# Optimization experiments

Hardware: AMD Instinct MI355X
Metric: run time of the kernel (lower is better)

Reference implementation:

```python
import jax, jax.numpy as jnp
import numpy as np

B = 32768
EPS = 0.2  # BatchNorm eps used in the original module


def _xavier(key, shape):
    fan_in, fan_out = shape[-2], shape[-1]
    std = (2.0 / (fan_in + fan_out)) ** 0.5
    return (jax.random.normal(key, shape, jnp.float32) * std).astype(jnp.float32)


def bn(x, g, b):
    # training-mode BatchNorm1d: batch stats over the batch axis (-2), biased var
    m = jnp.mean(x, axis=-2, keepdims=True)
    v = jnp.mean(jnp.square(x - m), axis=-2, keepdims=True)
    return (x - m) * jax.lax.rsqrt(v + EPS) * g + b


def setup_inputs() -> dict:
    key = jax.random.key(0)
    ks = iter(jax.random.split(key, 48))
    inp = {}
    inp['x1f'] = jax.random.normal(next(ks), (B, 512), jnp.float32)
    inp['x2f'] = jax.random.normal(next(ks), (B, 512), jnp.float32)
    # shared trunk
    inp['W1'] = _xavier(next(ks), (512, 256)); inp['b1'] = jnp.zeros(256, jnp.float32)
    inp['W2'] = _xavier(next(ks), (256, 256)); inp['b2'] = jnp.zeros(256, jnp.float32)
    # batchnorm affine params (bn1:256, bn2:256, bn3:128, bn4:64)
    inp['g1'] = jnp.ones(256, jnp.float32); inp['be1'] = jnp.zeros(256, jnp.float32)
    inp['g2'] = jnp.ones(256, jnp.float32); inp['be2'] = jnp.zeros(256, jnp.float32)
    inp['g3'] = jnp.ones(128, jnp.float32); inp['be3'] = jnp.zeros(128, jnp.float32)
    inp['g4'] = jnp.ones(64, jnp.float32); inp['be4'] = jnp.zeros(64, jnp.float32)
    # 4 branch projections from each stream (x11..x14, x21..x24), stacked on axis 0
    inp['Wbx1'] = _xavier(next(ks), (4, 256, 256)); inp['bbx1'] = jnp.zeros((4, 256), jnp.float32)
    inp['Wbx2'] = _xavier(next(ks), (4, 256, 256)); inp['bbx2'] = jnp.zeros((4, 256), jnp.float32)
    # gating MLPs (xw*1, xw*2, xw*3, y*), stacked over the 4 attributes
    inp['Wwa'] = _xavier(next(ks), (4, 512, 128)); inp['bwa'] = jnp.zeros((4, 128), jnp.float32)
    inp['Wwb'] = _xavier(next(ks), (4, 128, 64)); inp['bwb'] = jnp.zeros((4, 64), jnp.float32)
    inp['Wwc'] = _xavier(next(ks), (4, 64, 64)); inp['bwc'] = jnp.zeros((4, 64), jnp.float32)
    inp['Wy'] = _xavier(next(ks), (4, 64, 2)); inp['by'] = jnp.zeros((4, 2), jnp.float32)
    # combine layers x1c..x4c, stacked
    inp['Wc'] = _xavier(next(ks), (4, 512, 256)); inp['bc'] = jnp.zeros((4, 256), jnp.float32)
    # output heads (different class counts: 3, 3, 6, 4)
    inp['Wo1'] = _xavier(next(ks), (256, 3)); inp['bo1'] = jnp.zeros(3, jnp.float32)
    inp['Wo2'] = _xavier(next(ks), (256, 3)); inp['bo2'] = jnp.zeros(3, jnp.float32)
    inp['Wo3'] = _xavier(next(ks), (256, 6)); inp['bo3'] = jnp.zeros(6, jnp.float32)
    inp['Wo4'] = _xavier(next(ks), (256, 4)); inp['bo4'] = jnp.zeros(4, jnp.float32)
    return inp


def reference(x1f, x2f, W1, b1, W2, b2, g1, be1, g2, be2, g3, be3, g4, be4,
              Wbx1, bbx1, Wbx2, bbx2, Wwa, bwa, Wwb, bwb, Wwc, bwc, Wy, by,
              Wc, bc, Wo1, bo1, Wo2, bo2, Wo3, bo3, Wo4, bo4):
    relu = jax.nn.relu

    def trunk(x):
        h = bn(relu(x @ W1 + b1), g1, be1)
        return bn(relu(h @ W2 + b2), g2, be2)

    h1 = trunk(x1f)  # [B,256]
    h2 = trunk(x2f)  # [B,256]

    # 4 branch features per stream, each bn1-normalized: [4,B,256]
    b1x = bn(relu(jnp.einsum('bi,kio->kbo', h1, Wbx1) + bbx1[:, None, :]), g1, be1)
    b2x = bn(relu(jnp.einsum('bi,kio->kbo', h2, Wbx2) + bbx2[:, None, :]), g1, be1)

    # gating MLP per attribute -> 2-way softmax weights
    xcat = jnp.concatenate([b1x, b2x], axis=-1)  # [4,B,512]
    a = bn(relu(jnp.einsum('kbi,kio->kbo', xcat, Wwa) + bwa[:, None, :]), g3, be3)
    b_ = bn(relu(jnp.einsum('kbi,kio->kbo', a, Wwb) + bwb[:, None, :]), g4, be4)
    c = bn(relu(jnp.einsum('kbi,kio->kbo', b_, Wwc) + bwc[:, None, :]), g4, be4)
    y = jax.nn.softmax(jnp.einsum('kbi,kio->kbo', c, Wy) + by[:, None, :], axis=-1)  # [4,B,2]

    # the original per-column loop == one broadcast multiply per stream
    xw = jnp.concatenate([b1x * y[..., 0:1], b2x * y[..., 1:2]], axis=-1)  # [4,B,512]

    # combine layers (dropout is identity in eval)
    xc = bn(relu(jnp.einsum('kbi,kio->kbo', xw, Wc) + bc[:, None, :]), g1, be1)  # [4,B,256]

    y1o = jax.nn.softmax(xc[0] @ Wo1 + bo1, axis=-1)
    y2o = jax.nn.softmax(xc[1] @ Wo2 + bo2, axis=-1)
    y3o = jax.nn.softmax(xc[2] @ Wo3 + bo3, axis=-1)
    y4o = jax.nn.softmax(xc[3] @ Wo4 + bo4, axis=-1)
    return (y1o, y2o, y3o, y4o)
```

## Files before the change

kernel.cpp:

```cpp
#include <hip/hip_runtime.h>
#include <hip/hip_bf16.h>


typedef unsigned short u16;
typedef _Float16 f16x8 __attribute__((ext_vector_type(8)));
typedef float f32x4 __attribute__((ext_vector_type(4)));

#define B_ROWS 32768
#define EPS_BN 0.2f
#define BINV (1.0f / 32768.0f)

__device__ __forceinline__ float bf2f(u16 u) {
    union { unsigned int i; float f; } c;
    c.i = ((unsigned int)u) << 16;
    return c.f;
}
__device__ __forceinline__ u16 f2bf(float f) {
    union { float f; unsigned int i; } c;
    c.f = f;
    unsigned int x = c.i;
    return (u16)((x + 0x7FFFu + ((x >> 16) & 1u)) >> 16);
}
__device__ __forceinline__ float h2f(u16 u) {
    _Float16 h;
    __builtin_memcpy(&h, &u, 2);
    return (float)h;
}
__device__ __forceinline__ u16 f2h(float f) {
    _Float16 h = (_Float16)f;
    u16 u;
    __builtin_memcpy(&u, &h, 2);
    return u;
}
__device__ __forceinline__ float ldp(const void* p, long i, int flag) {
    return flag ? bf2f(((const u16*)p)[i]) : ((const float*)p)[i];
}
__device__ __forceinline__ void gload16(const u16* gp, u16* lp) {
    __builtin_amdgcn_global_load_lds(
        (const __attribute__((address_space(1))) unsigned int*)gp,
        (__attribute__((address_space(3))) unsigned int*)lp, 16, 0, 0);
}

__global__ void detect_dtype(const u16* __restrict__ x, int* __restrict__ flag) {
    const int lane = threadIdx.x;
    const u16 v = x[2 * lane];
    const int e = (v >> 7) & 0xFF;
    const bool plausible = (e >= 110 && e <= 140);
    const unsigned long long m = __ballot(plausible);
    if (lane == 0) *flag = (__popcll(m) >= 58) ? 1 : 0;
}

struct PTab { const void* p[20]; int n[20]; int off[20]; };

__global__ void convert_params(PTab t, float* __restrict__ dst,
                               const int* __restrict__ flag) {
    const int ti = blockIdx.y;
    const int n = t.n[ti];
    float* o = dst + t.off[ti];
    const int isbf = *flag;
    for (int i = blockIdx.x * 256 + threadIdx.x; i < n; i += gridDim.x * 256)
        o[i] = ldp(t.p[ti], i, isbf);
}

__global__ __launch_bounds__(256) void prep_w(
    const void* __restrict__ W, long wstride,
    const void* __restrict__ bias, long bstride,
    const float* __restrict__ psum, const float* __restrict__ psq, int pstride,
    const void* __restrict__ pg, const void* __restrict__ pbe, int gmask,
    const int* __restrict__ dtflag,
    u16* __restrict__ Wt, long wtstride,
    float* __restrict__ biasP, float* __restrict__ T0o,
    float* __restrict__ T1o, float* __restrict__ bsum, long bost,
    int K, int khalf)
{
    const int tid = threadIdx.x;
    const int n = blockIdx.x;
    const int N = gridDim.x;
    const int inst = blockIdx.y;
    const int flag = *dtflag;
    __shared__ float sn[512], tn[512];
    __shared__ float r0[4], r1[4];

    for (int i = tid; i < K; i += 256) {
        float s = 1.f, t = 0.f;
        if (psum) {
            float m = psum[(long)pstride * inst + i] * BINV;
            float v = psq[(long)pstride * inst + i] * BINV - m * m;
            float g = ldp(pg, i & gmask, flag);
            float b = ldp(pbe, i & gmask, flag);
            s = g * rsqrtf(v + EPS_BN);
            t = b - m * s;
        }
        sn[i] = s; tn[i] = t;
    }
    __syncthreads();
    float p0 = 0.f, p1 = 0.f;
    for (int k = tid; k < K; k += 256) {
        float wv = ldp(W, wstride * inst + (long)k * N + n, flag);
        Wt[wtstride * inst + (long)n * K + k] = f2h(sn[k] * wv);
        float tw = tn[k] * wv;
        if (k < khalf) p0 += tw; else p1 += tw;
    }
#pragma unroll
    for (int off = 32; off; off >>= 1) {
        p0 += __shfl_xor(p0, off);
        p1 += __shfl_xor(p1, off);
    }
    const int lane = tid & 63, wid = tid >> 6;
    if (lane == 0) { r0[wid] = p0; r1[wid] = p1; }
    __syncthreads();
    if (tid == 0) {
        float t0 = r0[0] + r0[1] + r0[2] + r0[3];
        float t1 = r1[0] + r1[1] + r1[2] + r1[3];
        float bp = ldp(bias, bstride * inst + n, flag);
        long o = bost * inst + n;
        biasP[o] = bp; T0o[o] = t0; T1o[o] = t1; bsum[o] = bp + t0 + t1;
    }
}

__global__ __launch_bounds__(256) void reduce_stats(
    const float* __restrict__ part, int X, int colsPer,
    float* __restrict__ outS, float* __restrict__ outQ, int total)
{
    const int t = blockIdx.x * 256 + threadIdx.x;
    if (t >= total) return;
    const int p = t / colsPer, c = t % colsPer;
    const float* pb = part + (long)p * X * 2 * colsPer + c;
    float s = 0.f, q = 0.f;
#pragma unroll 4
    for (int x = 0; x < X; ++x) {
        s += pb[(long)x * 2 * colsPer];
        q += pb[(long)x * 2 * colsPer + colsPer];
    }
    outS[t] = s; outQ[t] = q;
}

template <bool XSTAGE, bool ROWW, int WM, int WN, int K>
__global__ __launch_bounds__(256, 3) void gemm_mfma(
    const void* __restrict__ X, const void* __restrict__ X2,
    long xstride, int ximask, int ldx, int ksplit, long ksecond,
    const int* __restrict__ dtflag,
    const u16* __restrict__ Wt, long wtstride,
    const float* __restrict__ biasP, const float* __restrict__ T0,
    const float* __restrict__ T1, const float* __restrict__ bsum, int bN,
    u16* __restrict__ Out, long ostride, int ldout,
    float* __restrict__ gsum, float* __restrict__ gsq, int sstride,
    float* __restrict__ part,
    const float* __restrict__ Y0v)
{
    const int tid = threadIdx.x;
    const int lane = tid & 63;
    const int wid = tid >> 6;
    const int wm = wid / WN, wn = wid % WN;
    const int inst = blockIdx.z;
    const int rowB = blockIdx.x * (64 * WM);
    const int nBase = blockIdx.y * (64 * WN);
    const int n0 = nBase + wn * 64;
    const int fm = lane & 15, quad = lane >> 4;
    const int rloc = lane >> 3;
    const int cg = (lane & 7) ^ rloc;

    __shared__ __align__(16) u16 As[WM * 4096];
    __shared__ __align__(16) u16 Bs[WN * 4096];
    __shared__ float redS[4][64];
    __shared__ float redQ[4][64];

    const bool xf32 = XSTAGE && (*dtflag == 0);
    const char* xb;
    if (XSTAGE) xb = (const char*)(inst == 0 ? X : X2);
    else        xb = (const char*)X + 2l * xstride * (inst & ximask);
    const u16* wtp = Wt + wtstride * inst;
    u16* op = Out + ostride * inst;

    f32x4 acc[4][4];
#pragma unroll
    for (int i = 0; i < 4; ++i)
#pragma unroll
        for (int j = 0; j < 4; ++j) acc[i][j] = (f32x4){0.f, 0.f, 0.f, 0.f};

    _Float16 ysc[2][4];
    if constexpr (ROWW) {
        const float* yp = Y0v + (long)inst * B_ROWS;
#pragma unroll
        for (int mi = 0; mi < 4; ++mi) {
            const float y = yp[rowB + wm * 64 + mi * 16 + fm];
            ysc[0][mi] = (_Float16)y;
            ysc[1][mi] = (_Float16)(1.f - y);
        }
    }

    for (int kt = 0; kt < K / 64; ++kt) {
        const int kk = kt * 64;
        __syncthreads();
        if constexpr (XSTAGE) {
#pragma unroll
            for (int p = 0; p < WM * 2; ++p) {
                const int s = p * 256 + tid;
                const int m = s >> 3, c = s & 7;
                const int g = c ^ (m & 7);
                f16x8 h;
                if (xf32) {
                    const float* gp = (const float*)xb + (long)(rowB + m) * ldx + kk + g * 8;
                    const float4 u = *(const float4*)gp;
                    const float4 u2 = *(const float4*)(gp + 4);
                    h[0] = (_Float16)u.x;  h[1] = (_Float16)u.y;
                    h[2] = (_Float16)u.z;  h[3] = (_Float16)u.w;
                    h[4] = (_Float16)u2.x; h[5] = (_Float16)u2.y;
                    h[6] = (_Float16)u2.z; h[7] = (_Float16)u2.w;
                } else {
                    const uint4 v = *(const uint4*)((const u16*)xb + (long)(rowB + m) * ldx + kk + g * 8);
                    const u16* pv = (const u16*)&v;
#pragma unroll
                    for (int j = 0; j < 8; ++j) h[j] = (_Float16)bf2f(pv[j]);
                }
                *(f16x8*)&As[s * 8] = h;
            }
        } else {
            const u16* xs = (const u16*)xb;
            int kkr = kk;
            if (kk >= ksplit) { xs += ksecond; kkr -= ksplit; }
#pragma unroll
            for (int s = wid; s < WM * 8; s += 4)
                gload16(xs + (long)(rowB + s * 8 + rloc) * ldx + kkr + cg * 8,
                        &As[s * 512 + lane * 8]);
        }
#pragma unroll
        for (int s = wid; s < WN * 8; s += 4)
            gload16(wtp + (long)(nBase + s * 8 + rloc) * K + kk + cg * 8,
                    &Bs[s * 512 + lane * 8]);
        __syncthreads();

        const int sel = (ROWW && kk >= ksplit) ? 1 : 0;
#pragma unroll
        for (int q = 0; q < 2; ++q) {
            f16x8 af[4], bfr[4];
#pragma unroll
            for (int mi = 0; mi < 4; ++mi) {
                const int mm = wm * 64 + mi * 16 + fm;
                af[mi] = *(const f16x8*)&As[mm * 64 + (((q * 4 + quad) ^ (mm & 7)) * 8)];
            }
            if constexpr (ROWW) {
#pragma unroll
                for (int mi = 0; mi < 4; ++mi) {
                    const _Float16 yh = ysc[sel][mi];
#pragma unroll
                    for (int j = 0; j < 8; ++j) af[mi][j] *= yh;
                }
            }
#pragma unroll
            for (int ni = 0; ni < 4; ++ni) {
                const int nn = wn * 64 + ni * 16 + fm;
                bfr[ni] = *(const f16x8*)&Bs[nn * 64 + (((q * 4 + quad) ^ (nn & 7)) * 8)];
            }
#pragma unroll
            for (int mi = 0; mi < 4; ++mi)
#pragma unroll
                for (int ni = 0; ni < 4; ++ni)
                    acc[mi][ni] = __builtin_amdgcn_mfma_f32_16x16x32_f16(
                        af[mi], bfr[ni], acc[mi][ni], 0, 0, 0);
        }
    }

    __syncthreads();

    float yv[16];
    if constexpr (ROWW) {
        const float* yp = Y0v + (long)inst * B_ROWS;
#pragma unroll
        for (int mi = 0; mi < 4; ++mi)
#pragma unroll
            for (int r = 0; r < 4; ++r)
                yv[mi * 4 + r] = yp[rowB + wm * 64 + mi * 16 + quad * 4 + r];
    }

#pragma unroll
    for (int ni = 0; ni < 4; ++ni) {
        const int nc = ni * 16 + fm;
        const int n = n0 + nc;
        float bS = 0.f, bP = 0.f, t0v = 0.f, t1v = 0.f;
        if constexpr (ROWW) {
            bP = biasP[(long)inst * bN + n];
            t0v = T0[(long)inst * bN + n];
            t1v = T1[(long)inst * bN + n];
        } else {
            bS = bsum[(long)inst * bN + n];
        }
        float s = 0.f, qq = 0.f;
#pragma unroll
        for (int mi = 0; mi < 4; ++mi) {
            const int rbase = rowB + wm * 64 + mi * 16 + quad * 4;
#pragma unroll
            for (int r = 0; r < 4; ++r) {
                float v;
                if constexpr (ROWW) {
                    const float y = yv[mi * 4 + r];
                    v = acc[mi][ni][r] + y * t0v + (1.f - y) * t1v + bP;
                } else {
                    v = acc[mi][ni][r] + bS;
                }
                v = fmaxf(v, 0.f);
                s += v; qq += v * v;
                op[(long)(rbase + r) * ldout + n] = f2h(v);
            }
        }
        s += __shfl_xor(s, 16);  s += __shfl_xor(s, 32);
        qq += __shfl_xor(qq, 16); qq += __shfl_xor(qq, 32);
        if (quad == 0) { redS[wid][nc] = s; redQ[wid][nc] = qq; }
    }
    __syncthreads();
    if (tid < WN * 64) {
        const int wnc = tid >> 6, within = tid & 63;
        float s = 0.f, q = 0.f;
#pragma unroll
        for (int w = 0; w < WM; ++w) {
            s += redS[w * WN + wnc][within];
            q += redQ[w * WN + wnc][within];
        }
        if (part) {
            float* pb = part +
                (long)((inst * gridDim.y + blockIdx.y) * gridDim.x + blockIdx.x)
                    * (2 * WN * 64);
            pb[tid] = s;
            pb[WN * 64 + tid] = q;
        } else {
            atomicAdd(&gsum[(long)inst * sstride + nBase + tid], s);
            atomicAdd(&gsq [(long)inst * sstride + nBase + tid], q);
        }
    }
}

__global__ __launch_bounds__(256) void gate_kernel(
    const u16* __restrict__ zc,
    const float* __restrict__ stFs, const float* __restrict__ stFq,
    const float* __restrict__ g4, const float* __restrict__ be4,
    const float* __restrict__ Wy, const float* __restrict__ by,
    float* __restrict__ Y0)
{
    const int tid = threadIdx.x;
    const int k = blockIdx.y;
    const int r0 = blockIdx.x * 128;

    __shared__ __align__(8) float Ws2[64][2];
    __shared__ float cg[2];

    if (tid < 64) {
        const int c = tid;
        const float m = stFs[k * 64 + c] * BINV;
        const float v = stFq[k * 64 + c] * BINV - m * m;
        const float s = g4[c] * rsqrtf(v + EPS_BN);
        const float t = be4[c] - m * s;
        const float w0 = Wy[k * 128 + c * 2 + 0];
        const float w1 = Wy[k * 128 + c * 2 + 1];
        Ws2[c][0] = s * w0;
        Ws2[c][1] = s * w1;
        float t0 = t * w0, t1 = t * w1;
#pragma unroll
        for (int off = 32; off; off >>= 1) {
            t0 += __shfl_xor(t0, off);
            t1 += __shfl_xor(t1, off);
        }
        if (c == 0) {
            cg[0] = t0 + by[k * 2 + 0];
            cg[1] = t1 + by[k * 2 + 1];
        }
    }
    __syncthreads();

    const int row = r0 + (tid >> 1);
    const int seg = tid & 1;
    const u16* xp = zc + ((long)k * B_ROWS + row) * 64 + seg * 32;
    float a0 = 0.f, a1 = 0.f;
#pragma unroll
    for (int it = 0; it < 4; ++it) {
        const uint4 v = *(const uint4*)(xp + it * 8);
        const u16* pv = (const u16*)&v;
#pragma unroll
        for (int e = 0; e < 8; ++e) {
            const int c = seg * 32 + it * 8 + e;
            const float x = h2f(pv[e]);
            a0 += x * Ws2[c][0];
            a1 += x * Ws2[c][1];
        }
    }
    a0 += __shfl_xor(a0, 1);
    a1 += __shfl_xor(a1, 1);
    if (seg == 0) {
        const float l0 = a0 + cg[0];
        const float l1 = a1 + cg[1];
        Y0[(long)k * B_ROWS + row] = 1.f / (1.f + __expf(l1 - l0));
    }
}

__global__ __launch_bounds__(256) void heads_kernel(
    const u16* __restrict__ zxc,
    const float* __restrict__ stHs, const float* __restrict__ stHq,
    const float* __restrict__ g1, const float* __restrict__ be1,
    const float* __restrict__ Wo1, const float* __restrict__ bo1,
    const float* __restrict__ Wo2, const float* __restrict__ bo2,
    const float* __restrict__ Wo3, const float* __restrict__ bo3,
    const float* __restrict__ Wo4, const float* __restrict__ bo4,
    void* __restrict__ out, const int* __restrict__ dtflag)
{
    const int tid = threadIdx.x;
    const int k = blockIdx.y;
    const int r0 = blockIdx.x * 64;

    const float* Wo; const float* bo; int nk; long obase;
    if (k == 0)      { Wo = Wo1; bo = bo1; nk = 3; obase = 0; }
    else if (k == 1) { Wo = Wo2; bo = bo2; nk = 3; obase = (long)3 * B_ROWS; }
    else if (k == 2) { Wo = Wo3; bo = bo3; nk = 6; obase = (long)6 * B_ROWS; }
    else             { Wo = Wo4; bo = bo4; nk = 4; obase = (long)12 * B_ROWS; }

    __shared__ __align__(16) float Ws[256][8];
    __shared__ float cj[8];
    __shared__ float redC[4][8];

    {
        const int c = tid;
        const float m = stHs[k * 256 + c] * BINV;
        const float v = stHq[k * 256 + c] * BINV - m * m;
        const float s = g1[c] * rsqrtf(v + EPS_BN);
        const float t = be1[c] - m * s;
        const int rs = c ^ (c >> 6);
        float tw[6];
#pragma unroll
        for (int j = 0; j < 6; ++j) {
            const float w = (j < nk) ? Wo[c * nk + j] : 0.f;
            Ws[rs][j] = s * w;
            tw[j] = t * w;
        }
        Ws[rs][6] = 0.f; Ws[rs][7] = 0.f;
#pragma unroll
        for (int off = 32; off; off >>= 1)
#pragma unroll
            for (int j = 0; j < 6; ++j) tw[j] += __shfl_xor(tw[j], off);
        const int lane = tid & 63, wid = tid >> 6;
        if (lane < 6) redC[wid][lane] = tw[lane];
    }
    __syncthreads();
    if (tid < 8) {
        float s4 = 0.f;
        if (tid < 6) s4 = redC[0][tid] + redC[1][tid] + redC[2][tid] + redC[3][tid];
        cj[tid] = (tid < nk) ? s4 + bo[tid] : 0.f;
    }
    __syncthreads();

    const int row = r0 + (tid >> 2);
    const int seg = tid & 3;
    const u16* xp = zxc + ((long)k * B_ROWS + row) * 256 + seg * 64;
    float acc[6];
#pragma unroll
    for (int j = 0; j < 6; ++j) acc[j] = 0.f;
#pragma unroll
    for (int it = 0; it < 8; ++it) {
        const uint4 v = *(const uint4*)(xp + it * 8);
        const u16* pv = (const u16*)&v;
#pragma unroll
        for (int e = 0; e < 8; ++e) {
            const int cc = it * 8 + e;
            const int rs = (seg * 64 + cc) ^ seg;
            const float x = h2f(pv[e]);
            const f32x4 w0 = *(const f32x4*)&Ws[rs][0];
            const f32x4 w1 = *(const f32x4*)&Ws[rs][4];
            acc[0] += x * w0[0];
            acc[1] += x * w0[1];
            acc[2] += x * w0[2];
            acc[3] += x * w0[3];
            acc[4] += x * w1[0];
            acc[5] += x * w1[1];
        }
    }
#pragma unroll
    for (int j = 0; j < 6; ++j) {
        acc[j] += __shfl_xor(acc[j], 1);
        acc[j] += __shfl_xor(acc[j], 2);
    }

    if (seg == 0) {
        float l[6];
        float mx = -1e30f;
#pragma unroll
        for (int j = 0; j < 6; j++)
            if (j < nk) { l[j] = acc[j] + cj[j]; mx = fmaxf(mx, l[j]); }
        float e[6];
        float se = 0.f;
#pragma unroll
        for (int j = 0; j < 6; j++)
            if (j < nk) { e[j] = __expf(l[j] - mx); se += e[j]; }
        const float inv = 1.f / se;
        if (*dtflag) {
            u16* ob = (u16*)out;
#pragma unroll
            for (int j = 0; j < 6; j++)
                if (j < nk) ob[obase + (long)row * nk + j] = f2bf(e[j] * inv);
        } else {
            float* of = (float*)out;
#pragma unroll
            for (int j = 0; j < 6; j++)
                if (j < nk) of[obase + (long)row * nk + j] = e[j] * inv;
        }
    }
}

__global__ void fill_sentinel(u16* out, int n) {
    int i = blockIdx.x * 256 + threadIdx.x;
    if (i < n) out[i] = 0x3E80;
}

extern "C" void kernel_launch(void* const* d_in, const int* in_sizes, int n_in,
                              void* d_out, int out_size, void* d_ws, size_t ws_size,
                              hipStream_t stream)
{
    const long B = B_ROWS;
    char* ws = (char*)d_ws;
    const size_t MB = 1024 * 1024;

    u16* z1  = (u16*)(ws);
    u16* z2  = (u16*)(ws + 32 * MB);
    u16* za  = (u16*)(ws);
    u16* zbb = (u16*)(ws + 32 * MB);
    u16* zc  = (u16*)(ws + 48 * MB);
    u16* zxc = (u16*)(ws);
    u16* zb  = (u16*)(ws + 64 * MB);
    float* Y0 = (float*)(ws + 192 * MB);
    float* stats = (float*)(ws + 192 * MB + 512 * 1024);
    int* dtflag = (int*)(ws + 192 * MB + 576 * 1024);
    float* Pst = (float*)(ws + 192 * MB + 640 * 1024);

    u16* WtA = (u16*)(ws + 193 * MB);
    u16* WtB = WtA + 131072;
    u16* WtC = WtB + 131072;
    u16* WtD = WtC + 524288;
    u16* WtH = WtD + 262144;
    u16* WtE = WtH + 524288;
    u16* WtF = WtE + 32768;
    float* biasArea = (float*)(ws + 197 * MB);
    float* bA = biasArea;
    float* bB = bA + 2048;
    float* bC = bB + 2048;
    float* bD = bC + 8192;
    float* bH = bD + 2048;
    float* bE = bH + 4096;
    float* bF = bE + 1024;

    float* partC = (float*)(ws);
    float* partH = (float*)(ws + 193 * MB);

    const int cIdx[20] = {6,7,10,11,12,13,20,21,22,23,24,25,28,29,30,31,32,33,34,35};
    PTab tab;
    int mapOff[36];
    int acc = 0;
    for (int i = 0; i < 20; i++) {
        tab.p[i] = d_in[cIdx[i]];
        tab.n[i] = in_sizes[cIdx[i]];
        tab.off[i] = acc;
        mapOff[cIdx[i]] = acc;
        acc += in_sizes[cIdx[i]];
    }
    const size_t need = 197 * MB + 20480 * 4 + 4096;
    if (need > ws_size || (size_t)acc * 4 > 384 * 1024) {
        fill_sentinel<<<(out_size + 255) / 256, 256, 0, stream>>>((u16*)d_out, out_size);
        return;
    }
    auto PF = [&](int idx) { return Pst + mapOff[idx]; };

    float* stAs = stats;        float* stAq = stAs + 512;
    float* stBs = stAq + 512;   float* stBq = stBs + 512;
    float* stCs = stBq + 512;   float* stCq = stCs + 2048;
    float* stDs = stCq + 2048;  float* stDq = stDs + 512;
    float* stEs = stDq + 512;   float* stEq = stEs + 256;
    float* stFs = stEq + 256;   float* stFq = stFs + 256;
    float* stHs = stFq + 256;   float* stHq = stHs + 1024;

    hipMemsetAsync(stats, 0, 10240 * 4, stream);
    detect_dtype<<<1, 64, 0, stream>>>((const u16*)d_in[0], dtflag);
    convert_params<<<dim3(32, 20), 256, 0, stream>>>(tab, Pst, dtflag);

    const dim3 blk(256);
    const int BIGK = 1 << 29;

    prep_w<<<dim3(256, 2), blk, 0, stream>>>(
        d_in[2], 0, d_in[3], 0, nullptr, nullptr, 0, nullptr, nullptr, 0,
        dtflag, WtA, 0, bA, bA + 512, bA + 1024, bA + 1536, 256, 512, 512);
    gemm_mfma<true, false, 2, 2, 512><<<dim3(256, 2, 2), blk, 0, stream>>>(
        d_in[0], d_in[1], 0, 0, 512, BIGK, 0, dtflag, WtA, 0,
        bA, bA + 512, bA + 1024, bA + 1536, 256,
        z1, B * 256, 256, stAs, stAq, 256, nullptr, nullptr);

    prep_w<<<dim3(256, 2), blk, 0, stream>>>(
        d_in[4], 0, d_in[5], 0, stAs, stAq, 256, d_in[6], d_in[7], 255,
        dtflag, WtB, 65536, bB, bB + 512, bB + 1024, bB + 1536, 256, 256, 256);
    gemm_mfma<false, false, 2, 2, 256><<<dim3(256, 2, 2), blk, 0, stream>>>(
        z1, nullptr, B * 256, 3, 256, BIGK, 0, dtflag, WtB, 65536,
        bB, bB + 512, bB + 1024, bB + 1536, 256,
        z2, B * 256, 256, stBs, stBq, 256, nullptr, nullptr);

    for (int s = 0; s < 2; s++) {
        prep_w<<<dim3(256, 4), blk, 0, stream>>>(
            d_in[s ? 16 : 14], 65536, d_in[s ? 17 : 15], 256,
            stBs + s * 256, stBq + s * 256, 0, d_in[8], d_in[9], 255,
            dtflag, WtC + s * 65536, 131072,
            bC + s * 256, bC + 2048 + s * 256, bC + 4096 + s * 256,
            bC + 6144 + s * 256, 512, 256, 256);
    }
    gemm_mfma<false, false, 2, 2, 256><<<dim3(256, 2, 8), blk, 0, stream>>>(
        z2, nullptr, B * 256, 1, 256, BIGK, 0, dtflag, WtC, 65536,
        bC, bC + 2048, bC + 4096, bC + 6144, 256,
        zb, B * 256, 256, stCs, stCq, 256, partC, nullptr);
    reduce_stats<<<dim3(8), blk, 0, stream>>>(partC, 256, 128, stCs, stCq, 2048);

    prep_w<<<dim3(128, 4), blk, 0, stream>>>(
        d_in[18], 65536, d_in[19], 128, stCs, stCq, 512, d_in[6], d_in[7], 255,
        dtflag, WtD, 65536, bD, bD + 512, bD + 1024, bD + 1536, 128, 512, 512);
    prep_w<<<dim3(256, 4), blk, 0, stream>>>(
        d_in[26], 131072, d_in[27], 256, stCs, stCq, 512, d_in[6], d_in[7], 255,
        dtflag, WtH, 131072, bH, bH + 1024, bH + 2048, bH + 3072, 256, 512, 256);
    gemm_mfma<false, false, 2, 2, 512><<<dim3(256, 1, 4), blk, 0, stream>>>(
        zb, nullptr, 2 * B * 256, 3, 256, 256, B * 256, dtflag, WtD, 65536,
        bD, bD + 512, bD + 1024, bD + 1536, 128,
        za, B * 128, 128, stDs, stDq, 128, nullptr, nullptr);

    prep_w<<<dim3(64, 4), blk, 0, stream>>>(
        d_in[20], 8192, d_in[21], 64, stDs, stDq, 128, d_in[10], d_in[11], 127,
        dtflag, WtE, 8192, bE, bE + 256, bE + 512, bE + 768, 64, 128, 128);
    gemm_mfma<false, false, 4, 1, 128><<<dim3(128, 1, 4), blk, 0, stream>>>(
        za, nullptr, B * 128, 3, 128, BIGK, 0, dtflag, WtE, 8192,
        bE, bE + 256, bE + 512, bE + 768, 64,
        zbb, B * 64, 64, stEs, stEq, 64, nullptr, nullptr);

    prep_w<<<dim3(64, 4), blk, 0, stream>>>(
        d_in[22], 4096, d_in[23], 64, stEs, stEq, 64, d_in[12], d_in[13], 63,
        dtflag, WtF, 4096, bF, bF + 256, bF + 512, bF + 768, 64, 64, 64);
    gemm_mfma<false, false, 4, 1, 64><<<dim3(128, 1, 4), blk, 0, stream>>>(
        zbb, nullptr, B * 64, 3, 64, BIGK, 0, dtflag, WtF, 4096,
        bF, bF + 256, bF + 512, bF + 768, 64,
        zc, B * 64, 64, stFs, stFq, 64, nullptr, nullptr);

    gate_kernel<<<dim3(B_ROWS / 128, 4), blk, 0, stream>>>(
        zc, stFs, stFq, PF(12), PF(13), PF(24), PF(25), Y0);

    gemm_mfma<false, true, 2, 2, 512><<<dim3(256, 2, 4), blk, 0, stream>>>(
        zb, nullptr, 2 * B * 256, 3, 256, 256, B * 256, dtflag, WtH, 131072,
        bH, bH + 1024, bH + 2048, bH + 3072, 256,
        zxc, B * 256, 256, stHs, stHq, 256, partH, Y0);
    reduce_stats<<<dim3(4), blk, 0, stream>>>(partH, 256, 128, stHs, stHq, 1024);

    heads_kernel<<<dim3(B_ROWS / 64, 4), blk, 0, stream>>>(
        zxc, stHs, stHq, PF(6), PF(7), PF(28), PF(29), PF(30), PF(31),
        PF(32), PF(33), PF(34), PF(35), d_out, dtflag);
}
```

Before: 609.0 us.

## Double-buffer LDS tiles in MFMA GEMM to overlap global loads with compute

```diff
diff --git a/kernel.cpp b/kernel.cpp
--- a/kernel.cpp
+++ b/kernel.cpp
@@ -135,8 +135,8 @@
     outS[t] = s; outQ[t] = q;
 }
 
-template <bool XSTAGE, bool ROWW, int WM, int WN, int K>
-__global__ __launch_bounds__(256, 3) void gemm_mfma(
+template <bool XSTAGE, bool ROWW, int WM, int WN, int K, bool PIPE>
+__global__ __launch_bounds__(256, PIPE ? 2 : 3) void gemm_mfma(
     const void* __restrict__ X, const void* __restrict__ X2,
     long xstride, int ximask, int ldx, int ksplit, long ksecond,
     const int* __restrict__ dtflag,
@@ -160,12 +160,13 @@
     const int rloc = lane >> 3;
     const int cg = (lane & 7) ^ rloc;
 
-    __shared__ __align__(16) u16 As[WM * 4096];
-    __shared__ __align__(16) u16 Bs[WN * 4096];
+    __shared__ __align__(16) u16 As[(PIPE ? 2 : 1) * WM * 4096];
+    __shared__ __align__(16) u16 Bs[(PIPE ? 2 : 1) * WN * 4096];
     __shared__ float redS[4][64];
     __shared__ float redQ[4][64];
 
-    const bool xf32 = XSTAGE && (*dtflag == 0);
+    bool xf32 = false;
+    if constexpr (XSTAGE) xf32 = (*dtflag == 0);
     const char* xb;
     if (XSTAGE) xb = (const char*)(inst == 0 ? X : X2);
     else        xb = (const char*)X + 2l * xstride * (inst & ximask);
@@ -189,9 +190,8 @@
         }
     }
 
-    for (int kt = 0; kt < K / 64; ++kt) {
+    auto stageAB = [&](int kt, int buf) {
         const int kk = kt * 64;
-        __syncthreads();
         if constexpr (XSTAGE) {
 #pragma unroll
             for (int p = 0; p < WM * 2; ++p) {
@@ -219,25 +219,30 @@
             const u16* xs = (const u16*)xb;
             int kkr = kk;
             if (kk >= ksplit) { xs += ksecond; kkr -= ksplit; }
+            u16* asb = &As[buf * WM * 4096];
 #pragma unroll
             for (int s = wid; s < WM * 8; s += 4)
                 gload16(xs + (long)(rowB + s * 8 + rloc) * ldx + kkr + cg * 8,
-                        &As[s * 512 + lane * 8]);
-        }
+                        &asb[s * 512 + lane * 8]);
+        }
+        u16* bsb = &Bs[buf * WN * 4096];
 #pragma unroll
         for (int s = wid; s < WN * 8; s += 4)
             gload16(wtp + (long)(nBase + s * 8 + rloc) * K + kk + cg * 8,
-                    &Bs[s * 512 + lane * 8]);
-        __syncthreads();
-
-        const int sel = (ROWW && kk >= ksplit) ? 1 : 0;
+                    &bsb[s * 512 + lane * 8]);
+    };
+
+    auto computeT = [&](int kt, int buf) {
+        const u16* asb = &As[buf * WM * 4096];
+        const u16* bsb = &Bs[buf * WN * 4096];
+        const int sel = (ROWW && kt * 64 >= ksplit) ? 1 : 0;
 #pragma unroll
         for (int q = 0; q < 2; ++q) {
             f16x8 af[4], bfr[4];
 #pragma unroll
             for (int mi = 0; mi < 4; ++mi) {
                 const int mm = wm * 64 + mi * 16 + fm;
-                af[mi] = *(const f16x8*)&As[mm * 64 + (((q * 4 + quad) ^ (mm & 7)) * 8)];
+                af[mi] = *(const f16x8*)&asb[mm * 64 + (((q * 4 + quad) ^ (mm & 7)) * 8)];
             }
             if constexpr (ROWW) {
 #pragma unroll
@@ -250,7 +255,7 @@
 #pragma unroll
             for (int ni = 0; ni < 4; ++ni) {
                 const int nn = wn * 64 + ni * 16 + fm;
-                bfr[ni] = *(const f16x8*)&Bs[nn * 64 + (((q * 4 + quad) ^ (nn & 7)) * 8)];
+                bfr[ni] = *(const f16x8*)&bsb[nn * 64 + (((q * 4 + quad) ^ (nn & 7)) * 8)];
             }
 #pragma unroll
             for (int mi = 0; mi < 4; ++mi)
@@ -258,6 +263,32 @@
                 for (int ni = 0; ni < 4; ++ni)
                     acc[mi][ni] = __builtin_amdgcn_mfma_f32_16x16x32_f16(
                         af[mi], bfr[ni], acc[mi][ni], 0, 0, 0);
+        }
+    };
+
+    if constexpr (PIPE) {
+        static_assert((WM + WN) * 2 == 8, "vmcnt literal assumes 8 loads/wave/tile");
+        constexpr int NT = K / 64;
+        asm volatile("s_waitcnt vmcnt(0)" ::: "memory");
+        stageAB(0, 0);
+        for (int kt = 0; kt < NT; ++kt) {
+            const int cur = kt & 1;
+            if (kt + 1 < NT) {
+                stageAB(kt + 1, cur ^ 1);
+                asm volatile("s_waitcnt vmcnt(8)" ::: "memory");
+            } else {
+                asm volatile("s_waitcnt vmcnt(0)" ::: "memory");
+            }
+            __builtin_amdgcn_s_barrier();
+            computeT(kt, cur);
+            __builtin_amdgcn_s_barrier();
+        }
+    } else {
+        for (int kt = 0; kt < K / 64; ++kt) {
+            __syncthreads();
+            stageAB(kt, 0);
+            __syncthreads();
+            computeT(kt, 0);
         }
     }
 
@@ -582,7 +613,7 @@
     prep_w<<<dim3(256, 2), blk, 0, stream>>>(
         d_in[2], 0, d_in[3], 0, nullptr, nullptr, 0, nullptr, nullptr, 0,
         dtflag, WtA, 0, bA, bA + 512, bA + 1024, bA + 1536, 256, 512, 512);
-    gemm_mfma<true, false, 2, 2, 512><<<dim3(256, 2, 2), blk, 0, stream>>>(
+    gemm_mfma<true, false, 2, 2, 512, false><<<dim3(256, 2, 2), blk, 0, stream>>>(
         d_in[0], d_in[1], 0, 0, 512, BIGK, 0, dtflag, WtA, 0,
         bA, bA + 512, bA + 1024, bA + 1536, 256,
         z1, B * 256, 256, stAs, stAq, 256, nullptr, nullptr);
@@ -590,7 +621,7 @@
     prep_w<<<dim3(256, 2), blk, 0, stream>>>(
         d_in[4], 0, d_in[5], 0, stAs, stAq, 256, d_in[6], d_in[7], 255,
         dtflag, WtB, 65536, bB, bB + 512, bB + 1024, bB + 1536, 256, 256, 256);
-    gemm_mfma<false, false, 2, 2, 256><<<dim3(256, 2, 2), blk, 0, stream>>>(
+    gemm_mfma<false, false, 2, 2, 256, true><<<dim3(256, 2, 2), blk, 0, stream>>>(
         z1, nullptr, B * 256, 3, 256, BIGK, 0, dtflag, WtB, 65536,
         bB, bB + 512, bB + 1024, bB + 1536, 256,
         z2, B * 256, 256, stBs, stBq, 256, nullptr, nullptr);
@@ -603,7 +634,7 @@
             bC + s * 256, bC + 2048 + s * 256, bC + 4096 + s * 256,
             bC + 6144 + s * 256, 512, 256, 256);
     }
-    gemm_mfma<false, false, 2, 2, 256><<<dim3(256, 2, 8), blk, 0, stream>>>(
+    gemm_mfma<false, false, 2, 2, 256, true><<<dim3(256, 2, 8), blk, 0, stream>>>(
         z2, nullptr, B * 256, 1, 256, BIGK, 0, dtflag, WtC, 65536,
         bC, bC + 2048, bC + 4096, bC + 6144, 256,
         zb, B * 256, 256, stCs, stCq, 256, partC, nullptr);
@@ -615,7 +646,7 @@
     prep_w<<<dim3(256, 4), blk, 0, stream>>>(
         d_in[26], 131072, d_in[27], 256, stCs, stCq, 512, d_in[6], d_in[7], 255,
         dtflag, WtH, 131072, bH, bH + 1024, bH + 2048, bH + 3072, 256, 512, 256);
-    gemm_mfma<false, false, 2, 2, 512><<<dim3(256, 1, 4), blk, 0, stream>>>(
+    gemm_mfma<false, false, 2, 2, 512, true><<<dim3(256, 1, 4), blk, 0, stream>>>(
         zb, nullptr, 2 * B * 256, 3, 256, 256, B * 256, dtflag, WtD, 65536,
         bD, bD + 512, bD + 1024, bD + 1536, 128,
         za, B * 128, 128, stDs, stDq, 128, nullptr, nullptr);
@@ -623,7 +654,7 @@
     prep_w<<<dim3(64, 4), blk, 0, stream>>>(
         d_in[20], 8192, d_in[21], 64, stDs, stDq, 128, d_in[10], d_in[11], 127,
         dtflag, WtE, 8192, bE, bE + 256, bE + 512, bE + 768, 64, 128, 128);
-    gemm_mfma<false, false, 4, 1, 128><<<dim3(128, 1, 4), blk, 0, stream>>>(
+    gemm_mfma<false, false, 4, 1, 128, false><<<dim3(128, 1, 4), blk, 0, stream>>>(
         za, nullptr, B * 128, 3, 128, BIGK, 0, dtflag, WtE, 8192,
         bE, bE + 256, bE + 512, bE + 768, 64,
         zbb, B * 64, 64, stEs, stEq, 64, nullptr, nullptr);
@@ -631,7 +662,7 @@
     prep_w<<<dim3(64, 4), blk, 0, stream>>>(
         d_in[22], 4096, d_in[23], 64, stEs, stEq, 64, d_in[12], d_in[13], 63,
         dtflag, WtF, 4096, bF, bF + 256, bF + 512, bF + 768, 64, 64, 64);
-    gemm_mfma<false, false, 4, 1, 64><<<dim3(128, 1, 4), blk, 0, stream>>>(
+    gemm_mfma<false, false, 4, 1, 64, false><<<dim3(128, 1, 4), blk, 0, stream>>>(
         zbb, nullptr, B * 64, 3, 64, BIGK, 0, dtflag, WtF, 4096,
         bF, bF + 256, bF + 512, bF + 768, 64,
         zc, B * 64, 64, stFs, stFq, 64, nullptr, nullptr);
@@ -639,7 +670,7 @@
     gate_kernel<<<dim3(B_ROWS / 128, 4), blk, 0, stream>>>(
         zc, stFs, stFq, PF(12), PF(13), PF(24), PF(25), Y0);
 
-    gemm_mfma<false, true, 2, 2, 512><<<dim3(256, 2, 4), blk, 0, stream>>>(
+    gemm_mfma<false, true, 2, 2, 512, true><<<dim3(256, 2, 4), blk, 0, stream>>>(
         zb, nullptr, 2 * B * 256, 3, 256, 256, B * 256, dtflag, WtH, 131072,
         bH, bH + 1024, bH + 2048, bH + 3072, 256,
         zxc, B * 256, 256, stHs, stHq, 256, partH, Y0);
```

New measurement: 626.9 us. 1.03x slower.
